# Kernel optimization log

Hardware: AMD Instinct MI355X
Metric: run time of the kernel (lower is better)

## Reference

```python
import jax, jax.numpy as jnp
import numpy as np

B, S, L = 128, 16, 16          # batch, num_subsequences, subsequence_length (S == L by construction)
Z, HC, E = 512, 1024, 512      # z_dim, conductor_hidden_dim, embedding_dim
HD, V = 1024, 1024             # decoder_hidden_dim, vocab_size
T = S * L


def _lstm_layer(x_tbd, w_ih, w_hh, b_ih, b_hh):
    """Single LSTM layer over time. x_tbd: [T, B, D_in] -> hidden states [T, B, H].
    PyTorch gate order (i, f, g, o), zero initial state."""
    Tn, Bn, _ = x_tbd.shape
    H = w_hh.shape[1]
    gx = jnp.einsum('tbd,gd->tbg', x_tbd, w_ih) + (b_ih + b_hh)  # precompute input proj

    def step(carry, g):
        h, c = carry
        g = g + h @ w_hh.T
        i, f, gg, o = jnp.split(g, 4, axis=-1)
        c = jax.nn.sigmoid(f) * c + jax.nn.sigmoid(i) * jnp.tanh(gg)
        h = jax.nn.sigmoid(o) * jnp.tanh(c)
        return (h, c), h

    h0 = jnp.zeros((Bn, H), x_tbd.dtype)
    _, hs = jax.lax.scan(step, (h0, h0), gx)
    return hs


def setup_inputs() -> dict:
    key = jax.random.key(0)
    ks = jax.random.split(key, 20)
    s = 0.02
    return {
        'z': jax.random.normal(ks[0], (B, S, Z), jnp.float32),
        'x': jax.random.uniform(ks[1], (B, T, V), jnp.float32),
        'fcz_w': jax.random.normal(ks[2], (HC, Z), jnp.float32) * s,
        'fcz_b': jnp.zeros((HC,), jnp.float32),
        'c_wih': jax.random.normal(ks[3], (4 * HC, HC), jnp.float32) * s,
        'c_whh': jax.random.normal(ks[4], (4 * HC, HC), jnp.float32) * s,
        'c_bih': jnp.zeros((4 * HC,), jnp.float32),
        'c_bhh': jnp.zeros((4 * HC,), jnp.float32),
        'fcc_w': jax.random.normal(ks[5], (E, HC), jnp.float32) * s,
        'fcc_b': jnp.zeros((E,), jnp.float32),
        'd0_wih': jax.random.normal(ks[6], (4 * HD, V + E), jnp.float32) * s,
        'd0_whh': jax.random.normal(ks[7], (4 * HD, HD), jnp.float32) * s,
        'd0_bih': jnp.zeros((4 * HD,), jnp.float32),
        'd0_bhh': jnp.zeros((4 * HD,), jnp.float32),
        'd1_wih': jax.random.normal(ks[8], (4 * HD, HD), jnp.float32) * s,
        'd1_whh': jax.random.normal(ks[9], (4 * HD, HD), jnp.float32) * s,
        'd1_bih': jnp.zeros((4 * HD,), jnp.float32),
        'd1_bhh': jnp.zeros((4 * HD,), jnp.float32),
        'out_w': jax.random.normal(ks[10], (V, HD), jnp.float32) * s,
        'out_b': jnp.zeros((V,), jnp.float32),
    }


def reference(z, x, fcz_w, fcz_b, c_wih, c_whh, c_bih, c_bhh, fcc_w, fcc_b,
              d0_wih, d0_whh, d0_bih, d0_bhh, d1_wih, d1_whh, d1_bih, d1_bhh,
              out_w, out_b):
    # Conductor: fc_z then a 1-layer LSTM stepped over the S subsequence slots.
    cond_in = jnp.einsum('bsz,hz->bsh', z, fcz_w) + fcz_b          # [B, S, HC]
    cond_hs = _lstm_layer(cond_in.transpose(1, 0, 2), c_wih, c_whh, c_bih, c_bhh)  # [S, B, HC]
    emb = jnp.tanh(jnp.einsum('sbh,eh->sbe', cond_hs, fcc_w) + fcc_b)  # [S, B, E]
    emb = emb.transpose(1, 0, 2)                                   # [B, S, E]

    # Teacher forcing with S == L: prev_token at step k is x[:, k-1] (zeros at k=0).
    prev = jnp.concatenate([jnp.zeros((z.shape[0], 1, x.shape[-1]), x.dtype), x[:, :-1]], axis=1)  # [B, T, V]
    emb_rep = jnp.repeat(emb, L, axis=1)                           # [B, T, E]
    dec_in = jnp.concatenate([prev, emb_rep], axis=-1)             # [B, T, V+E]

    # 2-layer decoder LSTM (dropout inactive in eval), continuous state across subsequences.
    h0 = _lstm_layer(dec_in.transpose(1, 0, 2), d0_wih, d0_whh, d0_bih, d0_bhh)  # [T, B, HD]
    h1 = _lstm_layer(h0, d1_wih, d1_whh, d1_bih, d1_bhh)                        # [T, B, HD]
    logits = jnp.einsum('tbh,vh->tbv', h1, out_w) + out_b
    return logits.transpose(1, 0, 2)                               # [B, T, V]
```

## Files before the change

### kernel.cpp

```cpp
#include <hip/hip_runtime.h>


typedef float  floatx4 __attribute__((ext_vector_type(4)));
typedef __bf16 bf16x8  __attribute__((ext_vector_type(8)));
typedef unsigned short u16;

#define MFMA16(a, b, c) __builtin_amdgcn_mfma_f32_16x16x32_bf16(a, b, c, 0, 0, 0)

__device__ __forceinline__ u16 f2b(float f) {
  unsigned int u = __float_as_uint(f);
  u += 0x7fffu + ((u >> 16) & 1u);
  return (u16)(u >> 16);
}
__device__ __forceinline__ float sigf(float x) { return 1.f / (1.f + __expf(-x)); }
__device__ __forceinline__ float tanhf_fast(float x) {
  float e = __expf(-2.f * fabsf(x));
  float r = (1.f - e) / (1.f + e);
  return x >= 0.f ? r : -r;
}

__global__ void cast_f2b(const float* __restrict__ s, u16* __restrict__ d, int n4) {
  int i = blockIdx.x * blockDim.x + threadIdx.x;
  if (i < n4) {
    float4 v = ((const float4*)s)[i];
    u16* o = d + (size_t)i * 4;
    o[0] = f2b(v.x); o[1] = f2b(v.y); o[2] = f2b(v.z); o[3] = f2b(v.w);
  }
}

__global__ void cast_slice(const float* __restrict__ s, u16* __restrict__ d,
                           int sstride, int soff, int clog2) {
  int idx = blockIdx.x * blockDim.x + threadIdx.x;
  int r = idx >> clog2;
  int c = idx & ((1 << clog2) - 1);
  d[idx] = f2b(s[(size_t)r * sstride + soff + c]);
}

template <int AMODE, int SHIFT, int ACT>
__global__ __launch_bounds__(256) void gemm_kernel(
    const u16* __restrict__ A, const u16* __restrict__ W,
    const float* __restrict__ b1, const float* __restrict__ b2,
    float* __restrict__ Cf, u16* __restrict__ Cb,
    int M, int N, int K, int t0) {
  int tid = threadIdx.x;
  int lane = tid & 63, wave = tid >> 6;
  int lr = lane & 15, lk = (lane >> 4) * 8;
  int mblk = blockIdx.y * 128 + (wave >> 1) * 64;
  int nblk = blockIdx.x * 128 + (wave & 1) * 64;

  bf16x8 zf;
#pragma unroll
  for (int q = 0; q < 8; ++q) zf[q] = (__bf16)0.f;

  const u16* ap[4];
  bool aval[4];
#pragma unroll
  for (int i = 0; i < 4; ++i) {
    int r = mblk + i * 16 + lr;
    long arow;
    bool v = true;
    if (AMODE == 0) {
      arow = r;
    } else {
      int b = r >> 6, tt = r & 63;
      int t = t0 + tt;
      arow = (long)b * 256 + t - SHIFT;
      if (SHIFT && t == 0) { v = false; arow = 0; }
    }
    ap[i] = A + (size_t)arow * K + lk;
    aval[i] = v;
  }
  const u16* wp[4];
#pragma unroll
  for (int j = 0; j < 4; ++j) wp[j] = W + (size_t)(nblk + j * 16 + lr) * K + lk;

  floatx4 zero4 = {0.f, 0.f, 0.f, 0.f};
  floatx4 acc[4][4];
#pragma unroll
  for (int i = 0; i < 4; ++i)
#pragma unroll
    for (int j = 0; j < 4; ++j) acc[i][j] = zero4;

  for (int k = 0; k < K; k += 32) {
    bf16x8 av[4], bv[4];
#pragma unroll
    for (int i = 0; i < 4; ++i) {
      bf16x8 t = *(const bf16x8*)(ap[i] + k);
      if (AMODE == 1 && SHIFT) { if (!aval[i]) t = zf; }
      av[i] = t;
    }
#pragma unroll
    for (int j = 0; j < 4; ++j) bv[j] = *(const bf16x8*)(wp[j] + k);
#pragma unroll
    for (int i = 0; i < 4; ++i)
#pragma unroll
      for (int j = 0; j < 4; ++j) acc[i][j] = MFMA16(av[i], bv[j], acc[i][j]);
  }

#pragma unroll
  for (int i = 0; i < 4; ++i) {
    int rowb = mblk + i * 16 + (lane >> 4) * 4;
#pragma unroll
    for (int j = 0; j < 4; ++j) {
      int col = nblk + j * 16 + lr;
      float bias = 0.f;
      if (b1) bias += b1[col];
      if (b2) bias += b2[col];
#pragma unroll
      for (int r = 0; r < 4; ++r) {
        float v = acc[i][j][r] + bias;
        if (ACT == 1) v = tanhf_fast(v);
        size_t off = (size_t)(rowb + r) * N + col;
        if (Cf) Cf[off] = v;
        if (Cb) Cb[off] = f2b(v);
      }
    }
  }
}

__global__ __launch_bounds__(256) void lstm_step(
    const float* __restrict__ gx, int gx_bstride, int gx_off,
    const float* __restrict__ eadd, int e_bstride, int e_off,
    const u16* __restrict__ hp, int hp_bstride,
    const u16* __restrict__ Whh,
    float* __restrict__ c, int czero,
    u16* __restrict__ hout, int ho_bstride)
{
  __shared__ float G[4][64][17];
  int tid = threadIdx.x;
  int lane = tid & 63, wave = tid >> 6;
  int lr = lane & 15, lk = (lane >> 4) * 8;
  int wg = blockIdx.x;
  int mbase = (wg & 1) * 64;
  int j0 = (wg >> 1) * 16;
  int n0 = wave * 1024 + j0;

  floatx4 zero4 = {0.f, 0.f, 0.f, 0.f};
  floatx4 acc[4];
#pragma unroll
  for (int i = 0; i < 4; ++i) acc[i] = zero4;

  if (hp) {
    const u16* hpp[4];
#pragma unroll
    for (int i = 0; i < 4; ++i)
      hpp[i] = hp + (size_t)(mbase + i * 16 + lr) * hp_bstride + lk;
    const u16* wpp = Whh + (size_t)(n0 + lr) * 1024 + lk;
#pragma unroll 4
    for (int k = 0; k < 1024; k += 32) {
      bf16x8 bv = *(const bf16x8*)(wpp + k);
#pragma unroll
      for (int i = 0; i < 4; ++i) {
        bf16x8 av = *(const bf16x8*)(hpp[i] + k);
        acc[i] = MFMA16(av, bv, acc[i]);
      }
    }
  }

#pragma unroll
  for (int i = 0; i < 4; ++i) {
    int mloc = i * 16 + (lane >> 4) * 4;
    int col = n0 + lr;
#pragma unroll
    for (int r = 0; r < 4; ++r) {
      int b = mbase + mloc + r;
      float v = acc[i][r] + gx[(size_t)b * gx_bstride + gx_off + col];
      if (eadd) v += eadd[(size_t)b * e_bstride + e_off + col];
      G[wave][mloc + r][lr] = v;
    }
  }
  __syncthreads();

  for (int e = tid; e < 1024; e += 256) {
    int m = e >> 4, j = e & 15;
    int b = mbase + m, jj = j0 + j;
    float iv = G[0][m][j], fv = G[1][m][j], gv = G[2][m][j], ov = G[3][m][j];
    float cp = czero ? 0.f : c[(size_t)b * 1024 + jj];
    float cn = sigf(fv) * cp + sigf(iv) * tanhf_fast(gv);
    float h = sigf(ov) * tanhf_fast(cn);
    c[(size_t)b * 1024 + jj] = cn;
    hout[(size_t)b * ho_bstride + jj] = f2b(h);
  }
}

extern "C" void kernel_launch(void* const* d_in, const int* in_sizes, int n_in,
                              void* d_out, int out_size, void* d_ws, size_t ws_size,
                              hipStream_t stream) {
  const float* z      = (const float*)d_in[0];
  const float* x      = (const float*)d_in[1];
  const float* fcz_w  = (const float*)d_in[2];
  const float* fcz_b  = (const float*)d_in[3];
  const float* c_wih  = (const float*)d_in[4];
  const float* c_whh  = (const float*)d_in[5];
  const float* c_bih  = (const float*)d_in[6];
  const float* c_bhh  = (const float*)d_in[7];
  const float* fcc_w  = (const float*)d_in[8];
  const float* fcc_b  = (const float*)d_in[9];
  const float* d0_wih = (const float*)d_in[10];
  const float* d0_whh = (const float*)d_in[11];
  const float* d0_bih = (const float*)d_in[12];
  const float* d0_bhh = (const float*)d_in[13];
  const float* d1_wih = (const float*)d_in[14];
  const float* d1_whh = (const float*)d_in[15];
  const float* d1_bih = (const float*)d_in[16];
  const float* d1_bhh = (const float*)d_in[17];
  const float* out_w  = (const float*)d_in[18];
  const float* out_b  = (const float*)d_in[19];
  float* out = (float*)d_out;
  (void)in_sizes; (void)n_in; (void)out_size; (void)ws_size;

  char* ws = (char*)d_ws;
  size_t cur = 0;
  auto alloc = [&](size_t elems, size_t esz) -> void* {
    void* p = ws + cur;
    cur += (elems * esz + 255) & ~(size_t)255;
    return p;
  };
  u16*   wz      = (u16*)alloc(1024 * 512, 2);
  u16*   wcih    = (u16*)alloc(4096 * 1024, 2);
  u16*   wchh    = (u16*)alloc(4096 * 1024, 2);
  u16*   wfcc    = (u16*)alloc(512 * 1024, 2);
  u16*   w0v     = (u16*)alloc(4096 * 1024, 2);
  u16*   w0e     = (u16*)alloc(4096 * 512, 2);
  u16*   w0hh    = (u16*)alloc(4096 * 1024, 2);
  u16*   w1ih    = (u16*)alloc(4096 * 1024, 2);
  u16*   w1hh    = (u16*)alloc(4096 * 1024, 2);
  u16*   woutw   = (u16*)alloc(1024 * 1024, 2);
  u16*   zb      = (u16*)alloc(2048 * 512, 2);
  u16*   xb      = (u16*)alloc((size_t)32768 * 1024, 2);
  u16*   condinb = (u16*)alloc(2048 * 1024, 2);
  float* gxs     = (float*)alloc((size_t)2048 * 4096, 4);
  u16*   condh   = (u16*)alloc(2048 * 1024, 2);
  float* cc      = (float*)alloc(128 * 1024, 4);
  u16*   embb    = (u16*)alloc(2048 * 512, 2);
  float* gxbuf   = (float*)alloc((size_t)8192 * 4096, 4);
  u16*   h0b     = (u16*)alloc((size_t)32768 * 1024, 2);
  float* c0      = (float*)alloc(128 * 1024, 4);
  u16*   h1b     = (u16*)alloc((size_t)32768 * 1024, 2);
  float* c1      = (float*)alloc(128 * 1024, 4);

  auto cast = [&](const float* s, u16* d, size_t n) {
    cast_f2b<<<dim3((unsigned)(n / 1024)), dim3(256), 0, stream>>>(s, d, (int)(n / 4));
  };
  cast(fcz_w, wz, (size_t)1024 * 512);
  cast(c_wih, wcih, (size_t)4096 * 1024);
  cast(c_whh, wchh, (size_t)4096 * 1024);
  cast(fcc_w, wfcc, (size_t)512 * 1024);
  cast(d0_whh, w0hh, (size_t)4096 * 1024);
  cast(d1_wih, w1ih, (size_t)4096 * 1024);
  cast(d1_whh, w1hh, (size_t)4096 * 1024);
  cast(out_w, woutw, (size_t)1024 * 1024);
  cast(z, zb, (size_t)2048 * 512);
  cast(x, xb, (size_t)32768 * 1024);
  cast_slice<<<dim3(4096 * 1024 / 256), dim3(256), 0, stream>>>(d0_wih, w0v, 1536, 0, 10);
  cast_slice<<<dim3(4096 * 512 / 256), dim3(256), 0, stream>>>(d0_wih, w0e, 1536, 1024, 9);

  gemm_kernel<0, 0, 0><<<dim3(1024 / 128, 2048 / 128), dim3(256), 0, stream>>>(
      zb, wz, fcz_b, nullptr, nullptr, condinb, 2048, 1024, 512, 0);
  gemm_kernel<0, 0, 0><<<dim3(4096 / 128, 2048 / 128), dim3(256), 0, stream>>>(
      condinb, wcih, c_bih, c_bhh, gxs, nullptr, 2048, 4096, 1024, 0);
  for (int s = 0; s < 16; ++s) {
    const u16* hp = (s == 0) ? nullptr : condh + (size_t)(s - 1) * 1024;
    lstm_step<<<dim3(128), dim3(256), 0, stream>>>(
        gxs, 16 * 4096, s * 4096,
        nullptr, 0, 0,
        hp, 16 * 1024,
        wchh, cc, (s == 0) ? 1 : 0,
        condh + (size_t)s * 1024, 16 * 1024);
  }
  gemm_kernel<0, 0, 1><<<dim3(512 / 128, 2048 / 128), dim3(256), 0, stream>>>(
      condh, wfcc, fcc_b, nullptr, nullptr, embb, 2048, 512, 1024, 0);
  gemm_kernel<0, 0, 0><<<dim3(4096 / 128, 2048 / 128), dim3(256), 0, stream>>>(
      embb, w0e, nullptr, nullptr, gxs, nullptr, 2048, 4096, 512, 0);

  for (int ch = 0; ch < 4; ++ch) {
    gemm_kernel<1, 1, 0><<<dim3(4096 / 128, 8192 / 128), dim3(256), 0, stream>>>(
        xb, w0v, d0_bih, d0_bhh, gxbuf, nullptr, 8192, 4096, 1024, ch * 64);
    for (int tt = 0; tt < 64; ++tt) {
      int t = ch * 64 + tt;
      const u16* hp = (t == 0) ? nullptr : h0b + (size_t)(t - 1) * 1024;
      lstm_step<<<dim3(128), dim3(256), 0, stream>>>(
          gxbuf, 64 * 4096, tt * 4096,
          gxs, 16 * 4096, (t >> 4) * 4096,
          hp, 256 * 1024,
          w0hh, c0, (t == 0) ? 1 : 0,
          h0b + (size_t)t * 1024, 256 * 1024);
    }
  }
  for (int ch = 0; ch < 4; ++ch) {
    gemm_kernel<1, 0, 0><<<dim3(4096 / 128, 8192 / 128), dim3(256), 0, stream>>>(
        h0b, w1ih, d1_bih, d1_bhh, gxbuf, nullptr, 8192, 4096, 1024, ch * 64);
    for (int tt = 0; tt < 64; ++tt) {
      int t = ch * 64 + tt;
      const u16* hp = (t == 0) ? nullptr : h1b + (size_t)(t - 1) * 1024;
      lstm_step<<<dim3(128), dim3(256), 0, stream>>>(
          gxbuf, 64 * 4096, tt * 4096,
          nullptr, 0, 0,
          hp, 256 * 1024,
          w1hh, c1, (t == 0) ? 1 : 0,
          h1b + (size_t)t * 1024, 256 * 1024);
    }
  }
  gemm_kernel<0, 0, 0><<<dim3(1024 / 128, 32768 / 128), dim3(256), 0, stream>>>(
      h1b, woutw, out_b, nullptr, out, nullptr, 32768, 1024, 1024, 0);
}
```

Measured before the change: 18.36 ms.

## Replace per-timestep LSTM launches with persistent grid-barrier kernels and wavefront layer fusion

Replaces the per-timestep lstm_step launches (16 conductor steps plus 512 decoder steps) with persistent kernels that keep the cell state in registers and synchronise through an atomic grid barrier. Decoder layers 0 and 1 run together as a wavefront: layer 1 lags one step behind and uses a concatenated [W_ih|W_hh] weight, which removes the separate layer-1 input-projection GEMM. Hidden states go into an interleaved buffer that the output GEMM reads directly. This removes launch overhead and the serial ordering of the two layers, but it relies on all 64 or 128 blocks being co-resident for the spin barrier. Layer 1 also does a K=2048 matmul on each step.

```diff
diff --git a/kernel.cpp b/kernel.cpp
--- a/kernel.cpp
+++ b/kernel.cpp
@@ -17,6 +17,17 @@
   float e = __expf(-2.f * fabsf(x));
   float r = (1.f - e) / (1.f + e);
   return x >= 0.f ? r : -r;
+}
+
+__device__ __forceinline__ void gridbar(unsigned* bar, unsigned target) {
+  __syncthreads();
+  if (threadIdx.x == 0) {
+    __hip_atomic_fetch_add(bar, 1u, __ATOMIC_RELEASE, __HIP_MEMORY_SCOPE_AGENT);
+    while (__hip_atomic_load(bar, __ATOMIC_RELAXED, __HIP_MEMORY_SCOPE_AGENT) < target)
+      __builtin_amdgcn_s_sleep(2);
+    __builtin_amdgcn_fence(__ATOMIC_ACQUIRE, "agent");
+  }
+  __syncthreads();
 }
 
 __global__ void cast_f2b(const float* __restrict__ s, u16* __restrict__ d, int n4) {
@@ -28,12 +39,12 @@
   }
 }
 
-__global__ void cast_slice(const float* __restrict__ s, u16* __restrict__ d,
-                           int sstride, int soff, int clog2) {
+__global__ void cast_slice2(const float* __restrict__ s, u16* __restrict__ d,
+                            int sstride, int soff, int dstride, int doff, int clog2) {
   int idx = blockIdx.x * blockDim.x + threadIdx.x;
   int r = idx >> clog2;
   int c = idx & ((1 << clog2) - 1);
-  d[idx] = f2b(s[(size_t)r * sstride + soff + c]);
+  d[(size_t)r * dstride + doff + c] = f2b(s[(size_t)r * sstride + soff + c]);
 }
 
 template <int AMODE, int SHIFT, int ACT>
@@ -57,17 +68,19 @@
 #pragma unroll
   for (int i = 0; i < 4; ++i) {
     int r = mblk + i * 16 + lr;
-    long arow;
     bool v = true;
     if (AMODE == 0) {
-      arow = r;
-    } else {
+      ap[i] = A + (size_t)r * K + lk;
+    } else if (AMODE == 1) {
       int b = r >> 6, tt = r & 63;
       int t = t0 + tt;
-      arow = (long)b * 256 + t - SHIFT;
+      long arow = (long)b * 256 + t - SHIFT;
       if (SHIFT && t == 0) { v = false; arow = 0; }
-    }
-    ap[i] = A + (size_t)arow * K + lk;
+      ap[i] = A + (size_t)arow * K + lk;
+    } else {
+      int b = r >> 8, t = r & 255;
+      ap[i] = A + (size_t)(t + 1) * (128 * 2048) + (size_t)b * 2048 + 1024 + lk;
+    }
     aval[i] = v;
   }
   const u16* wp[4];
@@ -118,69 +131,171 @@
   }
 }
 
-__global__ __launch_bounds__(256) void lstm_step(
-    const float* __restrict__ gx, int gx_bstride, int gx_off,
-    const float* __restrict__ eadd, int e_bstride, int e_off,
-    const u16* __restrict__ hp, int hp_bstride,
-    const u16* __restrict__ Whh,
-    float* __restrict__ c, int czero,
-    u16* __restrict__ hout, int ho_bstride)
-{
-  __shared__ float G[4][64][17];
+__global__ __launch_bounds__(256) void cond_persist(
+    const float* __restrict__ gxs,
+    const u16* __restrict__ whh,
+    u16* __restrict__ condh,
+    unsigned* __restrict__ bar) {
   int tid = threadIdx.x;
-  int lane = tid & 63, wave = tid >> 6;
+  int lane = tid & 63, wv = tid >> 6;
+  int lr = lane & 15, lk = (lane >> 4) * 8;
+  int j0 = blockIdx.x * 16;
+  int j = j0 + lr;
+  int mbase = wv * 32;
+
+  const u16* wp[4];
+#pragma unroll
+  for (int g = 0; g < 4; ++g)
+    wp[g] = whh + (size_t)(g * 1024 + j0 + lr) * 1024 + lk;
+
+  float c[2][4];
+#pragma unroll
+  for (int i = 0; i < 2; ++i)
+#pragma unroll
+    for (int r = 0; r < 4; ++r) c[i][r] = 0.f;
+
+  for (int s = 0; s < 16; ++s) {
+    floatx4 acc[2][4];
+#pragma unroll
+    for (int i = 0; i < 2; ++i)
+#pragma unroll
+      for (int g = 0; g < 4; ++g) acc[i][g] = (floatx4){0.f, 0.f, 0.f, 0.f};
+    if (s > 0) {
+      const u16* a0 = condh + (size_t)((mbase + lr) * 16 + s - 1) * 1024 + lk;
+      const u16* a1 = condh + (size_t)((mbase + 16 + lr) * 16 + s - 1) * 1024 + lk;
+#pragma unroll 4
+      for (int k = 0; k < 1024; k += 32) {
+        bf16x8 av0 = *(const bf16x8*)(a0 + k);
+        bf16x8 av1 = *(const bf16x8*)(a1 + k);
+#pragma unroll
+        for (int g = 0; g < 4; ++g) {
+          bf16x8 bv = *(const bf16x8*)(wp[g] + k);
+          acc[0][g] = MFMA16(av0, bv, acc[0][g]);
+          acc[1][g] = MFMA16(av1, bv, acc[1][g]);
+        }
+      }
+    }
+#pragma unroll
+    for (int i = 0; i < 2; ++i)
+#pragma unroll
+      for (int r = 0; r < 4; ++r) {
+        int m = mbase + i * 16 + (lane >> 4) * 4 + r;
+        const float* gx = gxs + (size_t)(m * 16 + s) * 4096 + j;
+        float gi = acc[i][0][r] + gx[0];
+        float gf = acc[i][1][r] + gx[1024];
+        float gg = acc[i][2][r] + gx[2048];
+        float go = acc[i][3][r] + gx[3072];
+        float cn = sigf(gf) * c[i][r] + sigf(gi) * tanhf_fast(gg);
+        c[i][r] = cn;
+        condh[(size_t)(m * 16 + s) * 1024 + j] = f2b(sigf(go) * tanhf_fast(cn));
+      }
+    if (s < 15) gridbar(bar, 64u * (s + 1));
+  }
+}
+
+__global__ __launch_bounds__(256) void dec_persist(
+    const float* __restrict__ gxbuf,
+    const float* __restrict__ embgx,
+    const u16* __restrict__ w0hh,
+    const u16* __restrict__ wcat,
+    const float* __restrict__ b1i, const float* __restrict__ b1h,
+    u16* __restrict__ hsl,
+    float* __restrict__ c0g, float* __restrict__ c1g,
+    unsigned* __restrict__ bar, int t0) {
+  const size_t SL = 128 * 2048;
+  int tid = threadIdx.x;
+  int lane = tid & 63, wv = tid >> 6;
   int lr = lane & 15, lk = (lane >> 4) * 8;
   int wg = blockIdx.x;
-  int mbase = (wg & 1) * 64;
-  int j0 = (wg >> 1) * 16;
-  int n0 = wave * 1024 + j0;
-
-  floatx4 zero4 = {0.f, 0.f, 0.f, 0.f};
-  floatx4 acc[4];
-#pragma unroll
-  for (int i = 0; i < 4; ++i) acc[i] = zero4;
-
-  if (hp) {
-    const u16* hpp[4];
-#pragma unroll
-    for (int i = 0; i < 4; ++i)
-      hpp[i] = hp + (size_t)(mbase + i * 16 + lr) * hp_bstride + lk;
-    const u16* wpp = Whh + (size_t)(n0 + lr) * 1024 + lk;
+  const bool isL0 = wg < 64;
+  int u = isL0 ? wg : wg - 64;
+  int j0 = u * 16;
+  int j = j0 + lr;
+  int mbase = wv * 32;
+  const int KK = isL0 ? 1024 : 2048;
+  const u16* W = isL0 ? w0hh : wcat;
+
+  const u16* wp[4];
+#pragma unroll
+  for (int g = 0; g < 4; ++g)
+    wp[g] = W + (size_t)(g * 1024 + j0 + lr) * KK + lk;
+
+  float b1[4] = {0.f, 0.f, 0.f, 0.f};
+  if (!isL0) {
+#pragma unroll
+    for (int g = 0; g < 4; ++g) b1[g] = b1i[g * 1024 + j] + b1h[g * 1024 + j];
+  }
+
+  float* cg = isL0 ? c0g : c1g;
+  float c[2][4];
+#pragma unroll
+  for (int i = 0; i < 2; ++i)
+#pragma unroll
+    for (int r = 0; r < 4; ++r) {
+      int m = mbase + i * 16 + (lane >> 4) * 4 + r;
+      c[i][r] = (t0 == 0) ? 0.f : cg[(size_t)m * 1024 + j];
+    }
+
+  for (int p = 0; p <= 64; ++p) {
+    bool act = isL0 ? (p < 64) : (p >= 1);
+    if (act) {
+      int st = isL0 ? (t0 + p) : (t0 + p - 1);
+      floatx4 acc[2][4];
+#pragma unroll
+      for (int i = 0; i < 2; ++i)
+#pragma unroll
+        for (int g = 0; g < 4; ++g) acc[i][g] = (floatx4){0.f, 0.f, 0.f, 0.f};
+      if (!(isL0 && st == 0)) {
+        size_t base = isL0 ? (size_t)(st - 1) * SL : (size_t)st * SL;
+        const u16* a0 = hsl + base + (size_t)(mbase + lr) * 2048 + lk;
+        const u16* a1 = hsl + base + (size_t)(mbase + 16 + lr) * 2048 + lk;
 #pragma unroll 4
-    for (int k = 0; k < 1024; k += 32) {
-      bf16x8 bv = *(const bf16x8*)(wpp + k);
-#pragma unroll
-      for (int i = 0; i < 4; ++i) {
-        bf16x8 av = *(const bf16x8*)(hpp[i] + k);
-        acc[i] = MFMA16(av, bv, acc[i]);
+        for (int k = 0; k < KK; k += 32) {
+          bf16x8 av0 = *(const bf16x8*)(a0 + k);
+          bf16x8 av1 = *(const bf16x8*)(a1 + k);
+#pragma unroll
+          for (int g = 0; g < 4; ++g) {
+            bf16x8 bv = *(const bf16x8*)(wp[g] + k);
+            acc[0][g] = MFMA16(av0, bv, acc[0][g]);
+            acc[1][g] = MFMA16(av1, bv, acc[1][g]);
+          }
+        }
       }
-    }
-  }
-
-#pragma unroll
-  for (int i = 0; i < 4; ++i) {
-    int mloc = i * 16 + (lane >> 4) * 4;
-    int col = n0 + lr;
+#pragma unroll
+      for (int i = 0; i < 2; ++i)
+#pragma unroll
+        for (int r = 0; r < 4; ++r) {
+          int m = mbase + i * 16 + (lane >> 4) * 4 + r;
+          float gi, gf, gg, go;
+          if (isL0) {
+            const float* gx = gxbuf + (size_t)(m * 64 + p) * 4096 + j;
+            const float* eg = embgx + (size_t)(m * 16 + (st >> 4)) * 4096 + j;
+            gi = acc[i][0][r] + gx[0] + eg[0];
+            gf = acc[i][1][r] + gx[1024] + eg[1024];
+            gg = acc[i][2][r] + gx[2048] + eg[2048];
+            go = acc[i][3][r] + gx[3072] + eg[3072];
+          } else {
+            gi = acc[i][0][r] + b1[0];
+            gf = acc[i][1][r] + b1[1];
+            gg = acc[i][2][r] + b1[2];
+            go = acc[i][3][r] + b1[3];
+          }
+          float cn = sigf(gf) * c[i][r] + sigf(gi) * tanhf_fast(gg);
+          c[i][r] = cn;
+          u16 hb = f2b(sigf(go) * tanhf_fast(cn));
+          if (isL0) hsl[(size_t)st * SL + (size_t)m * 2048 + j] = hb;
+          else      hsl[(size_t)(st + 1) * SL + (size_t)m * 2048 + 1024 + j] = hb;
+        }
+    }
+    if (p < 64) gridbar(bar, 128u * (p + 1));
+  }
+#pragma unroll
+  for (int i = 0; i < 2; ++i)
 #pragma unroll
     for (int r = 0; r < 4; ++r) {
-      int b = mbase + mloc + r;
-      float v = acc[i][r] + gx[(size_t)b * gx_bstride + gx_off + col];
-      if (eadd) v += eadd[(size_t)b * e_bstride + e_off + col];
-      G[wave][mloc + r][lr] = v;
-    }
-  }
-  __syncthreads();
-
-  for (int e = tid; e < 1024; e += 256) {
-    int m = e >> 4, j = e & 15;
-    int b = mbase + m, jj = j0 + j;
-    float iv = G[0][m][j], fv = G[1][m][j], gv = G[2][m][j], ov = G[3][m][j];
-    float cp = czero ? 0.f : c[(size_t)b * 1024 + jj];
-    float cn = sigf(fv) * cp + sigf(iv) * tanhf_fast(gv);
-    float h = sigf(ov) * tanhf_fast(cn);
-    c[(size_t)b * 1024 + jj] = cn;
-    hout[(size_t)b * ho_bstride + jj] = f2b(h);
-  }
+      int m = mbase + i * 16 + (lane >> 4) * 4 + r;
+      cg[(size_t)m * 1024 + j] = c[i][r];
+    }
 }
 
 extern "C" void kernel_launch(void* const* d_in, const int* in_sizes, int n_in,
@@ -216,28 +331,29 @@
     cur += (elems * esz + 255) & ~(size_t)255;
     return p;
   };
-  u16*   wz      = (u16*)alloc(1024 * 512, 2);
-  u16*   wcih    = (u16*)alloc(4096 * 1024, 2);
-  u16*   wchh    = (u16*)alloc(4096 * 1024, 2);
-  u16*   wfcc    = (u16*)alloc(512 * 1024, 2);
-  u16*   w0v     = (u16*)alloc(4096 * 1024, 2);
-  u16*   w0e     = (u16*)alloc(4096 * 512, 2);
-  u16*   w0hh    = (u16*)alloc(4096 * 1024, 2);
-  u16*   w1ih    = (u16*)alloc(4096 * 1024, 2);
-  u16*   w1hh    = (u16*)alloc(4096 * 1024, 2);
-  u16*   woutw   = (u16*)alloc(1024 * 1024, 2);
-  u16*   zb      = (u16*)alloc(2048 * 512, 2);
-  u16*   xb      = (u16*)alloc((size_t)32768 * 1024, 2);
-  u16*   condinb = (u16*)alloc(2048 * 1024, 2);
-  float* gxs     = (float*)alloc((size_t)2048 * 4096, 4);
-  u16*   condh   = (u16*)alloc(2048 * 1024, 2);
-  float* cc      = (float*)alloc(128 * 1024, 4);
-  u16*   embb    = (u16*)alloc(2048 * 512, 2);
-  float* gxbuf   = (float*)alloc((size_t)8192 * 4096, 4);
-  u16*   h0b     = (u16*)alloc((size_t)32768 * 1024, 2);
-  float* c0      = (float*)alloc(128 * 1024, 4);
-  u16*   h1b     = (u16*)alloc((size_t)32768 * 1024, 2);
-  float* c1      = (float*)alloc(128 * 1024, 4);
+  u16*      wz      = (u16*)alloc(1024 * 512, 2);
+  u16*      wcih    = (u16*)alloc(4096 * 1024, 2);
+  u16*      wchh    = (u16*)alloc(4096 * 1024, 2);
+  u16*      wfcc    = (u16*)alloc(512 * 1024, 2);
+  u16*      w0v     = (u16*)alloc(4096 * 1024, 2);
+  u16*      w0e     = (u16*)alloc(4096 * 512, 2);
+  u16*      w0hh    = (u16*)alloc(4096 * 1024, 2);
+  u16*      wcat    = (u16*)alloc((size_t)4096 * 2048, 2);
+  u16*      woutw   = (u16*)alloc(1024 * 1024, 2);
+  u16*      zb      = (u16*)alloc(2048 * 512, 2);
+  u16*      xb      = (u16*)alloc((size_t)32768 * 1024, 2);
+  u16*      condinb = (u16*)alloc(2048 * 1024, 2);
+  float*    gxs     = (float*)alloc((size_t)2048 * 4096, 4);
+  u16*      condh   = (u16*)alloc(2048 * 1024, 2);
+  u16*      embb    = (u16*)alloc(2048 * 512, 2);
+  float*    gxbuf   = (float*)alloc((size_t)8192 * 4096, 4);
+  u16*      hsl     = (u16*)alloc((size_t)257 * 128 * 2048, 2);
+  float*    c0g     = (float*)alloc(128 * 1024, 4);
+  float*    c1g     = (float*)alloc(128 * 1024, 4);
+  unsigned* bar     = (unsigned*)alloc(128, 4);
+
+  hipMemsetAsync(bar, 0, 512, stream);
+  hipMemsetAsync(hsl, 0, (size_t)128 * 2048 * 2, stream);
 
   auto cast = [&](const float* s, u16* d, size_t n) {
     cast_f2b<<<dim3((unsigned)(n / 1024)), dim3(256), 0, stream>>>(s, d, (int)(n / 4));
@@ -247,27 +363,19 @@
   cast(c_whh, wchh, (size_t)4096 * 1024);
   cast(fcc_w, wfcc, (size_t)512 * 1024);
   cast(d0_whh, w0hh, (size_t)4096 * 1024);
-  cast(d1_wih, w1ih, (size_t)4096 * 1024);
-  cast(d1_whh, w1hh, (size_t)4096 * 1024);
   cast(out_w, woutw, (size_t)1024 * 1024);
   cast(z, zb, (size_t)2048 * 512);
   cast(x, xb, (size_t)32768 * 1024);
-  cast_slice<<<dim3(4096 * 1024 / 256), dim3(256), 0, stream>>>(d0_wih, w0v, 1536, 0, 10);
-  cast_slice<<<dim3(4096 * 512 / 256), dim3(256), 0, stream>>>(d0_wih, w0e, 1536, 1024, 9);
+  cast_slice2<<<dim3(4096 * 1024 / 256), dim3(256), 0, stream>>>(d0_wih, w0v, 1536, 0, 1024, 0, 10);
+  cast_slice2<<<dim3(4096 * 512 / 256), dim3(256), 0, stream>>>(d0_wih, w0e, 1536, 1024, 512, 0, 9);
+  cast_slice2<<<dim3(4096 * 1024 / 256), dim3(256), 0, stream>>>(d1_wih, wcat, 1024, 0, 2048, 0, 10);
+  cast_slice2<<<dim3(4096 * 1024 / 256), dim3(256), 0, stream>>>(d1_whh, wcat, 1024, 0, 2048, 1024, 10);
 
   gemm_kernel<0, 0, 0><<<dim3(1024 / 128, 2048 / 128), dim3(256), 0, stream>>>(
       zb, wz, fcz_b, nullptr, nullptr, condinb, 2048, 1024, 512, 0);
   gemm_kernel<0, 0, 0><<<dim3(4096 / 128, 2048 / 128), dim3(256), 0, stream>>>(
       condinb, wcih, c_bih, c_bhh, gxs, nullptr, 2048, 4096, 1024, 0);
-  for (int s = 0; s < 16; ++s) {
-    const u16* hp = (s == 0) ? nullptr : condh + (size_t)(s - 1) * 1024;
-    lstm_step<<<dim3(128), dim3(256), 0, stream>>>(
-        gxs, 16 * 4096, s * 4096,
-        nullptr, 0, 0,
-        hp, 16 * 1024,
-        wchh, cc, (s == 0) ? 1 : 0,
-        condh + (size_t)s * 1024, 16 * 1024);
-  }
+  cond_persist<<<dim3(64), dim3(256), 0, stream>>>(gxs, wchh, condh, bar);
   gemm_kernel<0, 0, 1><<<dim3(512 / 128, 2048 / 128), dim3(256), 0, stream>>>(
       condh, wfcc, fcc_b, nullptr, nullptr, embb, 2048, 512, 1024, 0);
   gemm_kernel<0, 0, 0><<<dim3(4096 / 128, 2048 / 128), dim3(256), 0, stream>>>(
@@ -276,31 +384,10 @@
   for (int ch = 0; ch < 4; ++ch) {
     gemm_kernel<1, 1, 0><<<dim3(4096 / 128, 8192 / 128), dim3(256), 0, stream>>>(
         xb, w0v, d0_bih, d0_bhh, gxbuf, nullptr, 8192, 4096, 1024, ch * 64);
-    for (int tt = 0; tt < 64; ++tt) {
-      int t = ch * 64 + tt;
-      const u16* hp = (t == 0) ? nullptr : h0b + (size_t)(t - 1) * 1024;
-      lstm_step<<<dim3(128), dim3(256), 0, stream>>>(
-          gxbuf, 64 * 4096, tt * 4096,
-          gxs, 16 * 4096, (t >> 4) * 4096,
-          hp, 256 * 1024,
-          w0hh, c0, (t == 0) ? 1 : 0,
-          h0b + (size_t)t * 1024, 256 * 1024);
-    }
-  }
-  for (int ch = 0; ch < 4; ++ch) {
-    gemm_kernel<1, 0, 0><<<dim3(4096 / 128, 8192 / 128), dim3(256), 0, stream>>>(
-        h0b, w1ih, d1_bih, d1_bhh, gxbuf, nullptr, 8192, 4096, 1024, ch * 64);
-    for (int tt = 0; tt < 64; ++tt) {
-      int t = ch * 64 + tt;
-      const u16* hp = (t == 0) ? nullptr : h1b + (size_t)(t - 1) * 1024;
-      lstm_step<<<dim3(128), dim3(256), 0, stream>>>(
-          gxbuf, 64 * 4096, tt * 4096,
-          nullptr, 0, 0,
-          hp, 256 * 1024,
-          w1hh, c1, (t == 0) ? 1 : 0,
-          h1b + (size_t)t * 1024, 256 * 1024);
-    }
-  }
-  gemm_kernel<0, 0, 0><<<dim3(1024 / 128, 32768 / 128), dim3(256), 0, stream>>>(
-      h1b, woutw, out_b, nullptr, out, nullptr, 32768, 1024, 1024, 0);
-}
+    dec_persist<<<dim3(128), dim3(256), 0, stream>>>(
+        gxbuf, gxs, w0hh, wcat, d1_bih, d1_bhh, hsl, c0g, c1g,
+        bar + 16 * (1 + ch), ch * 64);
+  }
+  gemm_kernel<2, 0, 0><<<dim3(1024 / 128, 32768 / 128), dim3(256), 0, stream>>>(
+      hsl, woutw, out_b, nullptr, out, nullptr, 32768, 1024, 1024, 0);
+}
```

After: 15.07 ms. -17.9%, faster.
